# Kernel tuning notes

Hardware: AMD Instinct MI355X
Metric: run time of the kernel (lower is better)

## Reference

```python
import jax, jax.numpy as jnp
import numpy as np

N, F_IN, HID, C, E = 100000, 1024, 16, 64, 3200000
BN_EPS = 1e-5


def setup_inputs() -> dict:
    key = jax.random.key(0)
    ks = jax.random.split(key, 8)
    x = jax.random.normal(ks[0], (N, F_IN), jnp.float32)
    edge_index = jax.random.randint(ks[1], (2, E), 0, N, dtype=jnp.int32)
    w1 = jax.random.normal(ks[2], (F_IN, HID), jnp.float32) / np.float32(np.sqrt(F_IN))
    b1 = jnp.zeros((HID,), jnp.float32)
    w2 = jax.random.normal(ks[3], (HID, C), jnp.float32) / np.float32(np.sqrt(HID))
    b2 = jnp.zeros((C,), jnp.float32)
    mlp_w = jax.random.normal(ks[4], (C, C), jnp.float32) / np.float32(np.sqrt(C))
    mlp_b = jnp.zeros((C,), jnp.float32)
    bn_gamma = jnp.ones((C,), jnp.float32)
    bn_beta = jnp.zeros((C,), jnp.float32)
    # per-node channel weight param, xavier_normal_ init on shape (N, 1)
    xavier_std = np.float32(np.sqrt(2.0 / (N + 1)))
    weight_raw = jax.random.normal(ks[5], (N, 1), jnp.float32) * xavier_std
    return {"x": x, "edge_index": edge_index, "w1": w1, "b1": b1, "w2": w2,
            "b2": b2, "mlp_w": mlp_w, "mlp_b": mlp_b, "bn_gamma": bn_gamma,
            "bn_beta": bn_beta, "weight_raw": weight_raw}


def _gcn_norm(edge_index, n):
    # PyG GCNConv default: add self-loops, norm = deg^-1/2[src] * deg^-1/2[dst]
    loop = jnp.arange(n, dtype=edge_index.dtype)
    src = jnp.concatenate([edge_index[0], loop])
    dst = jnp.concatenate([edge_index[1], loop])
    deg = jax.ops.segment_sum(jnp.ones_like(dst, dtype=jnp.float32), dst, num_segments=n)
    dis = jax.lax.rsqrt(jnp.maximum(deg, 1.0))  # deg >= 1 with self-loops
    norm = dis[src] * dis[dst]
    return src, dst, norm


def _gcn_conv(h, src, dst, norm, w, b, n):
    h = h @ w                              # [N, out] dense transform first
    msg = h[src] * norm[:, None]           # gather + scale per edge
    out = jax.ops.segment_sum(msg, dst, num_segments=n)  # scatter-add
    return out + b


def reference(x, edge_index, w1, b1, w2, b2, mlp_w, mlp_b, bn_gamma, bn_beta, weight_raw):
    n = x.shape[0]
    src, dst, norm = _gcn_norm(edge_index, n)
    h = _gcn_conv(x, src, dst, norm, w1, b1, n)
    h = jax.nn.relu(h)                     # dropout is identity in eval mode
    h = _gcn_conv(h, src, dst, norm, w2, b2, n)
    h = jax.nn.log_softmax(h, axis=1)
    h = jnp.exp(weight_raw) * h            # exp(xavier param) channel weight
    h = h @ mlp_w + mlp_b                  # final MLP (C*1 -> C)
    mean = jnp.mean(h, axis=0)
    var = jnp.mean(jnp.square(h - mean), axis=0)  # biased var, BN training stats
    h = (h - mean) * jax.lax.rsqrt(var + BN_EPS) * bn_gamma + bn_beta
    return jax.nn.log_softmax(h, axis=1)
```

## Files before the change

kernel.cpp:

```cpp
#include <hip/hip_runtime.h>
#include <math.h>

#define NN   100000
#define FIN  1024
#define HIDN 16
#define CCH  64
#define EE   3200000
#define BNEPS 1e-5f
#define NB   ((NN + 255) / 256)
#define NPART 8
#define PSZ  (NN / NPART)

__global__ __launch_bounds__(256) void k_hist(const int* __restrict__ ei,
                                              unsigned* __restrict__ deg) {
  int p = blockIdx.x & 7;
  int blk = blockIdx.x >> 3;
  int nblk = gridDim.x >> 3;
  int lo = p * PSZ, hi = lo + PSZ;
  for (int e = blk * 256 + threadIdx.x; e < EE; e += nblk * 256) {
    int d = ei[EE + e];
    if (d >= lo && d < hi) atomicAdd(&deg[d], 1u);
  }
}

__global__ __launch_bounds__(256) void k_scan_part(const unsigned* __restrict__ deg,
                                                   unsigned* __restrict__ exc,
                                                   unsigned* __restrict__ bsum) {
  __shared__ unsigned s[256];
  int t = threadIdx.x, i = blockIdx.x * 256 + t;
  unsigned v = (i < NN) ? deg[i] : 0u;
  s[t] = v;
  __syncthreads();
#pragma unroll
  for (int off = 1; off < 256; off <<= 1) {
    unsigned u = (t >= off) ? s[t - off] : 0u;
    __syncthreads();
    s[t] += u;
    __syncthreads();
  }
  if (i < NN) exc[i] = s[t] - v;
  if (t == 255) bsum[blockIdx.x] = s[255];
}

__global__ __launch_bounds__(512) void k_scan_boff(const unsigned* __restrict__ bsum,
                                                   unsigned* __restrict__ boff) {
  __shared__ unsigned s[512];
  int t = threadIdx.x;
  unsigned v = (t < NB) ? bsum[t] : 0u;
  s[t] = v;
  __syncthreads();
#pragma unroll
  for (int off = 1; off < 512; off <<= 1) {
    unsigned u = (t >= off) ? s[t - off] : 0u;
    __syncthreads();
    s[t] += u;
    __syncthreads();
  }
  if (t < NB) boff[t] = s[t] - v;
}

__global__ __launch_bounds__(256) void k_scan_final(const unsigned* __restrict__ exc,
                                                    const unsigned* __restrict__ boff,
                                                    const unsigned* __restrict__ deg,
                                                    int* __restrict__ rowptr,
                                                    int* __restrict__ cur,
                                                    float* __restrict__ dis) {
  int i = blockIdx.x * 256 + threadIdx.x;
  if (i < NN) {
    int r = (int)(boff[i >> 8] + exc[i]);
    rowptr[i] = r;
    cur[i] = r;
    dis[i] = rsqrtf((float)(deg[i] + 1u));
  } else if (i == NN) {
    rowptr[NN] = EE;
  }
}

__global__ __launch_bounds__(256) void k_place(const int* __restrict__ ei,
                                               int* __restrict__ cur,
                                               int* __restrict__ perm) {
  int p = blockIdx.x & 7;
  int blk = blockIdx.x >> 3;
  int nblk = gridDim.x >> 3;
  int lo = p * PSZ, hi = lo + PSZ;
  for (int e = blk * 256 + threadIdx.x; e < EE; e += nblk * 256) {
    int d = ei[EE + e];
    if (d >= lo && d < hi) {
      int s = ei[e];
      int slot = atomicAdd(&cur[d], 1);
      perm[slot] = s;
    }
  }
}

#define G1_ROWS_PER_BLOCK 128
__global__ __launch_bounds__(256, 2) void k_gemm1(const float* __restrict__ x,
                                                  const float* __restrict__ w1,
                                                  const float* __restrict__ dis,
                                                  float* __restrict__ xw1s) {
  __shared__ __align__(16) float w1s[1024 * 16];
  const float4* w1v = (const float4*)w1;
  for (int idx = threadIdx.x; idx < 4096; idx += 256) {
    int k = idx >> 2, qj = idx & 3;
    int pq = qj ^ ((k >> 1) & 3);
    *(float4*)&w1s[(k << 4) + (pq << 2)] = w1v[idx];
  }
  __syncthreads();

  const int lane = threadIdx.x & 63;
  const int wave = threadIdx.x >> 6;
  const int sw = (lane >> 1) & 3;
  const int wave_row0 = blockIdx.x * G1_ROWS_PER_BLOCK + wave * 32;

  for (int g = 0; g < 8; ++g) {
    int row0 = wave_row0 + g * 4;
    if (row0 >= NN) break;
    int r0 = row0;
    int r1 = min(row0 + 1, NN - 1);
    int r2 = min(row0 + 2, NN - 1);
    int r3 = min(row0 + 3, NN - 1);

    const float* p0 = x + (size_t)r0 * FIN + lane;
    const float* p1 = x + (size_t)r1 * FIN + lane;
    const float* p2 = x + (size_t)r2 * FIN + lane;
    const float* p3 = x + (size_t)r3 * FIN + lane;

    float xa[16], xb[16], xc[16], xd[16];
#pragma unroll
    for (int i = 0; i < 16; ++i) {
      xa[i] = __builtin_nontemporal_load(p0 + i * 64);
      xb[i] = __builtin_nontemporal_load(p1 + i * 64);
      xc[i] = __builtin_nontemporal_load(p2 + i * 64);
      xd[i] = __builtin_nontemporal_load(p3 + i * 64);
    }

    float acc[64];
#pragma unroll
    for (int t = 0; t < 64; ++t) acc[t] = 0.0f;

#pragma unroll
    for (int i = 0; i < 16; ++i) {
      const float* wr = &w1s[(i * 64 + lane) << 4];
      float xv0 = xa[i], xv1 = xb[i], xv2 = xc[i], xv3 = xd[i];
#pragma unroll
      for (int q = 0; q < 4; ++q) {
        float4 wq = *(const float4*)(wr + ((q ^ sw) << 2));
        int b = q * 4;
        acc[b + 0]      += xv0 * wq.x;
        acc[b + 1]      += xv0 * wq.y;
        acc[b + 2]      += xv0 * wq.z;
        acc[b + 3]      += xv0 * wq.w;
        acc[16 + b + 0] += xv1 * wq.x;
        acc[16 + b + 1] += xv1 * wq.y;
        acc[16 + b + 2] += xv1 * wq.z;
        acc[16 + b + 3] += xv1 * wq.w;
        acc[32 + b + 0] += xv2 * wq.x;
        acc[32 + b + 1] += xv2 * wq.y;
        acc[32 + b + 2] += xv2 * wq.z;
        acc[32 + b + 3] += xv2 * wq.w;
        acc[48 + b + 0] += xv3 * wq.x;
        acc[48 + b + 1] += xv3 * wq.y;
        acc[48 + b + 2] += xv3 * wq.z;
        acc[48 + b + 3] += xv3 * wq.w;
      }
    }

#pragma unroll
    for (int o = 32; o >= 1; o >>= 1) {
      bool up = (lane & o) != 0;
#pragma unroll
      for (int t = 0; t < o; ++t) {
        float send = up ? acc[t] : acc[t + o];
        float recv = __shfl_xor(send, o, 64);
        float keep = up ? acc[t + o] : acc[t];
        acc[t] = keep + recv;
      }
    }

    int grow = row0 + (lane >> 4);
    if (grow < NN) xw1s[grow * HIDN + (lane & 15)] = acc[0] * dis[grow];
  }
}

template <int MODE>
__global__ __launch_bounds__(256) void k_agg(const int* __restrict__ rowptr,
                                             const int* __restrict__ perm,
                                             const float* __restrict__ dis,
                                             const float* __restrict__ sfs,
                                             const float* __restrict__ b1,
                                             float* __restrict__ out) {
  int g = blockIdx.x * 4 + (threadIdx.x >> 6);
  if (g >= NN) return;
  int lane = threadIdx.x & 63;
  int eo = lane >> 4;
  int j = lane & 15;
  int beg = rowptr[g], end = rowptr[g + 1];
  float acc0 = 0.0f, acc1 = 0.0f;
  int e = beg + eo;
  for (; e + 4 < end; e += 8) {
    int s0 = perm[e];
    int s1 = perm[e + 4];
    acc0 += sfs[(size_t)s0 * HIDN + j];
    acc1 += sfs[(size_t)s1 * HIDN + j];
  }
  if (e < end) acc0 += sfs[(size_t)perm[e] * HIDN + j];
  float acc = acc0 + acc1;
  acc += __shfl_xor(acc, 16, 64);
  acc += __shfl_xor(acc, 32, 64);
  if (eo == 0) {
    float di = dis[g];
    float v = di * (acc + sfs[(size_t)g * HIDN + j]);
    if (MODE == 0)
      out[(size_t)g * HIDN + j] = fmaxf(v + b1[j], 0.0f) * di;
    else
      out[(size_t)g * HIDN + j] = v;
  }
}

__global__ __launch_bounds__(256) void k_fuse2(const float* __restrict__ agg2,
                                               const float* __restrict__ w2,
                                               const float* __restrict__ b2,
                                               const float* __restrict__ mlpw,
                                               const float* __restrict__ mlpb,
                                               const float* __restrict__ wraw,
                                               float* __restrict__ out,
                                               double* __restrict__ gsum,
                                               double* __restrict__ gsq) {
  __shared__ __align__(16) float2 w2p[8 * CCH];
  __shared__ __align__(16) float2 mlpp[32 * CCH];
  __shared__ __align__(16) float avbuf[4][HIDN];
  __shared__ __align__(16) float gbuf[4][CCH];
  __shared__ double reds[256];
  __shared__ double redq[256];
  for (int idx = threadIdx.x; idx < 8 * CCH; idx += 256) {
    int k2 = idx >> 6, j = idx & 63;
    w2p[idx] = make_float2(w2[(2 * k2) * CCH + j], w2[(2 * k2 + 1) * CCH + j]);
  }
  for (int idx = threadIdx.x; idx < 32 * CCH; idx += 256) {
    int c2 = idx >> 6, j = idx & 63;
    mlpp[idx] = make_float2(mlpw[(2 * c2) * CCH + j], mlpw[(2 * c2 + 1) * CCH + j]);
  }
  __syncthreads();

  const int lane = threadIdx.x & 63;
  const int wave = threadIdx.x >> 6;
  const int j = lane;
  const float b2j = b2[j];
  const float mbj = mlpb[j];
  const int gw = blockIdx.x * 4 + wave;
  const int nw = gridDim.x * 4;

  double sum = 0.0, sq = 0.0;
  for (int i = gw; i < NN; i += nw) {
    float av = agg2[(size_t)i * HIDN + (lane & 15)];
    if (lane < HIDN) avbuf[wave][lane] = av;

    float2 h2p = make_float2(0.0f, 0.0f);
#pragma unroll
    for (int k2 = 0; k2 < 8; ++k2) {
      float2 a = *(const float2*)&avbuf[wave][2 * k2];
      float2 wv = w2p[k2 * CCH + j];
      h2p.x = fmaf(a.x, wv.x, h2p.x);
      h2p.y = fmaf(a.y, wv.y, h2p.y);
    }
    float h2 = h2p.x + h2p.y + b2j;

    float mx = h2;
#pragma unroll
    for (int o = 32; o >= 1; o >>= 1) mx = fmaxf(mx, __shfl_xor(mx, o, 64));
    float ex = __expf(h2 - mx);
    float se = ex;
#pragma unroll
    for (int o = 32; o >= 1; o >>= 1) se += __shfl_xor(se, o, 64);
    float lsm = h2 - mx - __logf(se);

    float gg = __expf(wraw[i]) * lsm;
    gbuf[wave][j] = gg;

    float2 mp = make_float2(0.0f, 0.0f);
#pragma unroll
    for (int c2 = 0; c2 < 32; ++c2) {
      float2 gv = *(const float2*)&gbuf[wave][2 * c2];
      float2 wv = mlpp[c2 * CCH + j];
      mp.x = fmaf(gv.x, wv.x, mp.x);
      mp.y = fmaf(gv.y, wv.y, mp.y);
    }
    float m = mp.x + mp.y + mbj;

    out[(size_t)i * CCH + j] = m;
    sum += (double)m;
    sq = fma((double)m, (double)m, sq);
  }

  reds[threadIdx.x] = sum;
  redq[threadIdx.x] = sq;
  __syncthreads();
  if (threadIdx.x < 64) {
    double s = reds[threadIdx.x] + reds[threadIdx.x + 64] +
               reds[threadIdx.x + 128] + reds[threadIdx.x + 192];
    double q = redq[threadIdx.x] + redq[threadIdx.x + 64] +
               redq[threadIdx.x + 128] + redq[threadIdx.x + 192];
    atomicAdd(&gsum[threadIdx.x], s);
    atomicAdd(&gsq[threadIdx.x], q);
  }
}

__global__ void k_stats(const double* __restrict__ gsum,
                        const double* __restrict__ gsq,
                        const float* __restrict__ gamma,
                        const float* __restrict__ beta,
                        float* __restrict__ bnp) {
  int j = threadIdx.x;
  if (j >= CCH) return;
  const double inv_n = 1.0 / (double)NN;
  double mean = gsum[j] * inv_n;
  double var = gsq[j] * inv_n - mean * mean;
  float sc = (float)(rsqrt(var + (double)BNEPS)) * gamma[j];
  bnp[j] = (float)mean;
  bnp[CCH + j] = sc;
  bnp[2 * CCH + j] = beta[j];
}

__global__ __launch_bounds__(256) void k_out(float* __restrict__ out,
                                             const float* __restrict__ bnp) {
  const int lane = threadIdx.x & 63;
  const int wave = threadIdx.x >> 6;
  const int j = lane;
  const float mean = bnp[j];
  const float sc = bnp[CCH + j];
  const float bt = bnp[2 * CCH + j];
  const int gw = blockIdx.x * 4 + wave;
  const int nw = gridDim.x * 4;
  for (int i = gw; i < NN; i += nw) {
    float m = out[(size_t)i * CCH + j];
    float y = fmaf(m - mean, sc, bt);
    float mx = y;
#pragma unroll
    for (int o = 32; o >= 1; o >>= 1) mx = fmaxf(mx, __shfl_xor(mx, o, 64));
    float ex = __expf(y - mx);
    float se = ex;
#pragma unroll
    for (int o = 32; o >= 1; o >>= 1) se += __shfl_xor(se, o, 64);
    out[(size_t)i * CCH + j] = y - mx - __logf(se);
  }
}

extern "C" void kernel_launch(void* const* d_in, const int* in_sizes, int n_in,
                              void* d_out, int out_size, void* d_ws, size_t ws_size,
                              hipStream_t stream) {
  const float* x     = (const float*)d_in[0];
  const int*   ei    = (const int*)d_in[1];
  const float* w1    = (const float*)d_in[2];
  const float* b1    = (const float*)d_in[3];
  const float* w2    = (const float*)d_in[4];
  const float* b2    = (const float*)d_in[5];
  const float* mlpw  = (const float*)d_in[6];
  const float* mlpb  = (const float*)d_in[7];
  const float* gamma = (const float*)d_in[8];
  const float* beta  = (const float*)d_in[9];
  const float* wraw  = (const float*)d_in[10];
  float* out = (float*)d_out;

  char* w = (char*)d_ws;
  size_t off = 0;
  auto take = [&](size_t bytes) -> void* {
    void* p = w + off;
    off = (off + bytes + 255) & ~(size_t)255;
    return p;
  };
  unsigned* deg    = (unsigned*)take((size_t)NN * 4);
  float*    dis    = (float*)take((size_t)NN * 4);
  unsigned* exc    = (unsigned*)take((size_t)NN * 4);
  unsigned* bsum   = (unsigned*)take((size_t)NB * 4);
  unsigned* boff   = (unsigned*)take((size_t)NB * 4);
  int*      rowptr = (int*)take((size_t)(NN + 1) * 4);
  int*      cur    = (int*)take((size_t)NN * 4);
  int*      perm   = (int*)take((size_t)EE * 4);
  float*    xw1s   = (float*)take((size_t)NN * HIDN * 4);
  float*    rh1s   = (float*)take((size_t)NN * HIDN * 4);
  float*    agg2   = (float*)take((size_t)NN * HIDN * 4);
  double*   gsum   = (double*)take(CCH * 8);
  double*   gsq    = (double*)take(CCH * 8);
  float*    bnp    = (float*)take(3 * CCH * 4);
  (void)ws_size; (void)n_in; (void)in_sizes; (void)out_size;

  hipMemsetAsync(deg, 0, (size_t)NN * 4, stream);
  hipMemsetAsync(gsum, 0, CCH * 8, stream);
  hipMemsetAsync(gsq, 0, CCH * 8, stream);

  k_hist<<<2048, 256, 0, stream>>>(ei, deg);
  k_scan_part<<<NB, 256, 0, stream>>>(deg, exc, bsum);
  k_scan_boff<<<1, 512, 0, stream>>>(bsum, boff);
  k_scan_final<<<(NN + 256) / 256 + 1, 256, 0, stream>>>(exc, boff, deg, rowptr, cur, dis);
  k_place<<<2048, 256, 0, stream>>>(ei, cur, perm);

  k_gemm1<<<(NN + G1_ROWS_PER_BLOCK - 1) / G1_ROWS_PER_BLOCK, 256, 0, stream>>>(
      x, w1, dis, xw1s);
  k_agg<0><<<(NN + 3) / 4, 256, 0, stream>>>(rowptr, perm, dis, xw1s, b1, rh1s);
  k_agg<1><<<(NN + 3) / 4, 256, 0, stream>>>(rowptr, perm, dis, rh1s, b1, agg2);
  k_fuse2<<<2048, 256, 0, stream>>>(agg2, w2, b2, mlpw, mlpb, wraw, out, gsum, gsq);
  k_stats<<<1, 64, 0, stream>>>(gsum, gsq, gamma, beta, bnp);
  k_out<<<1024, 256, 0, stream>>>(out, bnp);
}
```

Baseline: 593.6 us.

## Split gemm1 K dimension into two passes, unroll aggregation loop, enlarge grids

The dense x@w1 kernel is split into two launches, each covering half of the 1024-wide K dimension. Each launch uses half the LDS for weights and half the register-held x values. The first writes partial sums to a new buffer, and the second adds them and applies the degree scaling. The gather-aggregation loop is unrolled to four independent accumulators for more memory-level parallelism, and the fuse2 and output kernels get larger grids. The split adds a partial-sum round trip and an extra launch, and x is still read once overall, in two strided halves.

```diff
diff --git a/kernel.cpp b/kernel.cpp
--- a/kernel.cpp
+++ b/kernel.cpp
@@ -94,16 +94,18 @@
 }
 
 #define G1_ROWS_PER_BLOCK 128
+template <int HALF>
 __global__ __launch_bounds__(256, 2) void k_gemm1(const float* __restrict__ x,
                                                   const float* __restrict__ w1,
                                                   const float* __restrict__ dis,
+                                                  float* __restrict__ part,
                                                   float* __restrict__ xw1s) {
-  __shared__ __align__(16) float w1s[1024 * 16];
+  __shared__ __align__(16) float w1s[512 * 16];
   const float4* w1v = (const float4*)w1;
-  for (int idx = threadIdx.x; idx < 4096; idx += 256) {
+  for (int idx = threadIdx.x; idx < 2048; idx += 256) {
     int k = idx >> 2, qj = idx & 3;
     int pq = qj ^ ((k >> 1) & 3);
-    *(float4*)&w1s[(k << 4) + (pq << 2)] = w1v[idx];
+    *(float4*)&w1s[(k << 4) + (pq << 2)] = w1v[HALF * 2048 + idx];
   }
   __syncthreads();
 
@@ -120,14 +122,14 @@
     int r2 = min(row0 + 2, NN - 1);
     int r3 = min(row0 + 3, NN - 1);
 
-    const float* p0 = x + (size_t)r0 * FIN + lane;
-    const float* p1 = x + (size_t)r1 * FIN + lane;
-    const float* p2 = x + (size_t)r2 * FIN + lane;
-    const float* p3 = x + (size_t)r3 * FIN + lane;
-
-    float xa[16], xb[16], xc[16], xd[16];
-#pragma unroll
-    for (int i = 0; i < 16; ++i) {
+    const float* p0 = x + (size_t)r0 * FIN + HALF * 512 + lane;
+    const float* p1 = x + (size_t)r1 * FIN + HALF * 512 + lane;
+    const float* p2 = x + (size_t)r2 * FIN + HALF * 512 + lane;
+    const float* p3 = x + (size_t)r3 * FIN + HALF * 512 + lane;
+
+    float xa[8], xb[8], xc[8], xd[8];
+#pragma unroll
+    for (int i = 0; i < 8; ++i) {
       xa[i] = __builtin_nontemporal_load(p0 + i * 64);
       xb[i] = __builtin_nontemporal_load(p1 + i * 64);
       xc[i] = __builtin_nontemporal_load(p2 + i * 64);
@@ -139,7 +141,7 @@
     for (int t = 0; t < 64; ++t) acc[t] = 0.0f;
 
 #pragma unroll
-    for (int i = 0; i < 16; ++i) {
+    for (int i = 0; i < 8; ++i) {
       const float* wr = &w1s[(i * 64 + lane) << 4];
       float xv0 = xa[i], xv1 = xb[i], xv2 = xc[i], xv3 = xd[i];
 #pragma unroll
@@ -178,7 +180,14 @@
     }
 
     int grow = row0 + (lane >> 4);
-    if (grow < NN) xw1s[grow * HIDN + (lane & 15)] = acc[0] * dis[grow];
+    if (grow < NN) {
+      int oidx = grow * HIDN + (lane & 15);
+      if (HALF == 0) {
+        part[oidx] = acc[0];
+      } else {
+        xw1s[oidx] = (part[oidx] + acc[0]) * dis[grow];
+      }
+    }
   }
 }
 
@@ -195,16 +204,20 @@
   int eo = lane >> 4;
   int j = lane & 15;
   int beg = rowptr[g], end = rowptr[g + 1];
-  float acc0 = 0.0f, acc1 = 0.0f;
+  float acc0 = 0.0f, acc1 = 0.0f, acc2 = 0.0f, acc3 = 0.0f;
   int e = beg + eo;
-  for (; e + 4 < end; e += 8) {
+  for (; e + 12 < end; e += 16) {
     int s0 = perm[e];
     int s1 = perm[e + 4];
+    int s2 = perm[e + 8];
+    int s3 = perm[e + 12];
     acc0 += sfs[(size_t)s0 * HIDN + j];
     acc1 += sfs[(size_t)s1 * HIDN + j];
-  }
-  if (e < end) acc0 += sfs[(size_t)perm[e] * HIDN + j];
-  float acc = acc0 + acc1;
+    acc2 += sfs[(size_t)s2 * HIDN + j];
+    acc3 += sfs[(size_t)s3 * HIDN + j];
+  }
+  for (; e < end; e += 4) acc0 += sfs[(size_t)perm[e] * HIDN + j];
+  float acc = (acc0 + acc1) + (acc2 + acc3);
   acc += __shfl_xor(acc, 16, 64);
   acc += __shfl_xor(acc, 32, 64);
   if (eo == 0) {
@@ -376,6 +389,7 @@
   int*      rowptr = (int*)take((size_t)(NN + 1) * 4);
   int*      cur    = (int*)take((size_t)NN * 4);
   int*      perm   = (int*)take((size_t)EE * 4);
+  float*    partb  = (float*)take((size_t)NN * HIDN * 4);
   float*    xw1s   = (float*)take((size_t)NN * HIDN * 4);
   float*    rh1s   = (float*)take((size_t)NN * HIDN * 4);
   float*    agg2   = (float*)take((size_t)NN * HIDN * 4);
@@ -394,11 +408,13 @@
   k_scan_final<<<(NN + 256) / 256 + 1, 256, 0, stream>>>(exc, boff, deg, rowptr, cur, dis);
   k_place<<<2048, 256, 0, stream>>>(ei, cur, perm);
 
-  k_gemm1<<<(NN + G1_ROWS_PER_BLOCK - 1) / G1_ROWS_PER_BLOCK, 256, 0, stream>>>(
-      x, w1, dis, xw1s);
+  const int g1grid = (NN + G1_ROWS_PER_BLOCK - 1) / G1_ROWS_PER_BLOCK;
+  k_gemm1<0><<<g1grid, 256, 0, stream>>>(x, w1, dis, partb, xw1s);
+  k_gemm1<1><<<g1grid, 256, 0, stream>>>(x, w1, dis, partb, xw1s);
+
   k_agg<0><<<(NN + 3) / 4, 256, 0, stream>>>(rowptr, perm, dis, xw1s, b1, rh1s);
   k_agg<1><<<(NN + 3) / 4, 256, 0, stream>>>(rowptr, perm, dis, rh1s, b1, agg2);
-  k_fuse2<<<2048, 256, 0, stream>>>(agg2, w2, b2, mlpw, mlpb, wraw, out, gsum, gsq);
+  k_fuse2<<<4096, 256, 0, stream>>>(agg2, w2, b2, mlpw, mlpb, wraw, out, gsum, gsq);
   k_stats<<<1, 64, 0, stream>>>(gsum, gsq, gamma, beta, bnp);
-  k_out<<<1024, 256, 0, stream>>>(out, bnp);
-}
+  k_out<<<2048, 256, 0, stream>>>(out, bnp);
+}
```

Result: slower. 622.4 us (+4.8%).

## Pad w1 LDS layout, unroll aggregation gathers deeper, enlarge fuse/out grids

Applied to the files above, without the earlier changes.

The first GEMM now stores w1 in shared memory with a row stride of 17 floats and reads scalars instead of XOR-swizzled float4 vectors. This avoids bank conflicts through padding but issues four times as many LDS reads. The aggregation kernel now keeps four independent gather accumulators per lane instead of two, so more irregular loads are in flight, and its tail loop handles the remainder. The grids for k_fuse2 and k_out are doubled to add parallelism.

```diff
diff --git a/kernel.cpp b/kernel.cpp
--- a/kernel.cpp
+++ b/kernel.cpp
@@ -94,22 +94,20 @@
 }
 
 #define G1_ROWS_PER_BLOCK 128
+#define W1LD 17
 __global__ __launch_bounds__(256, 2) void k_gemm1(const float* __restrict__ x,
                                                   const float* __restrict__ w1,
                                                   const float* __restrict__ dis,
                                                   float* __restrict__ xw1s) {
-  __shared__ __align__(16) float w1s[1024 * 16];
-  const float4* w1v = (const float4*)w1;
-  for (int idx = threadIdx.x; idx < 4096; idx += 256) {
-    int k = idx >> 2, qj = idx & 3;
-    int pq = qj ^ ((k >> 1) & 3);
-    *(float4*)&w1s[(k << 4) + (pq << 2)] = w1v[idx];
+  __shared__ float w1s[1024 * W1LD];
+  for (int idx = threadIdx.x; idx < 1024 * 16; idx += 256) {
+    int k = idx >> 4, j = idx & 15;
+    w1s[k * W1LD + j] = w1[idx];
   }
   __syncthreads();
 
   const int lane = threadIdx.x & 63;
   const int wave = threadIdx.x >> 6;
-  const int sw = (lane >> 1) & 3;
   const int wave_row0 = blockIdx.x * G1_ROWS_PER_BLOCK + wave * 32;
 
   for (int g = 0; g < 8; ++g) {
@@ -140,28 +138,15 @@
 
 #pragma unroll
     for (int i = 0; i < 16; ++i) {
-      const float* wr = &w1s[(i * 64 + lane) << 4];
+      const float* wr = &w1s[(i * 64 + lane) * W1LD];
       float xv0 = xa[i], xv1 = xb[i], xv2 = xc[i], xv3 = xd[i];
 #pragma unroll
-      for (int q = 0; q < 4; ++q) {
-        float4 wq = *(const float4*)(wr + ((q ^ sw) << 2));
-        int b = q * 4;
-        acc[b + 0]      += xv0 * wq.x;
-        acc[b + 1]      += xv0 * wq.y;
-        acc[b + 2]      += xv0 * wq.z;
-        acc[b + 3]      += xv0 * wq.w;
-        acc[16 + b + 0] += xv1 * wq.x;
-        acc[16 + b + 1] += xv1 * wq.y;
-        acc[16 + b + 2] += xv1 * wq.z;
-        acc[16 + b + 3] += xv1 * wq.w;
-        acc[32 + b + 0] += xv2 * wq.x;
-        acc[32 + b + 1] += xv2 * wq.y;
-        acc[32 + b + 2] += xv2 * wq.z;
-        acc[32 + b + 3] += xv2 * wq.w;
-        acc[48 + b + 0] += xv3 * wq.x;
-        acc[48 + b + 1] += xv3 * wq.y;
-        acc[48 + b + 2] += xv3 * wq.z;
-        acc[48 + b + 3] += xv3 * wq.w;
+      for (int j = 0; j < 16; ++j) {
+        float wv = wr[j];
+        acc[j]      += xv0 * wv;
+        acc[16 + j] += xv1 * wv;
+        acc[32 + j] += xv2 * wv;
+        acc[48 + j] += xv3 * wv;
       }
     }
 
@@ -195,16 +180,20 @@
   int eo = lane >> 4;
   int j = lane & 15;
   int beg = rowptr[g], end = rowptr[g + 1];
-  float acc0 = 0.0f, acc1 = 0.0f;
+  float acc0 = 0.0f, acc1 = 0.0f, acc2 = 0.0f, acc3 = 0.0f;
   int e = beg + eo;
-  for (; e + 4 < end; e += 8) {
+  for (; e + 12 < end; e += 16) {
     int s0 = perm[e];
     int s1 = perm[e + 4];
+    int s2 = perm[e + 8];
+    int s3 = perm[e + 12];
     acc0 += sfs[(size_t)s0 * HIDN + j];
     acc1 += sfs[(size_t)s1 * HIDN + j];
-  }
-  if (e < end) acc0 += sfs[(size_t)perm[e] * HIDN + j];
-  float acc = acc0 + acc1;
+    acc2 += sfs[(size_t)s2 * HIDN + j];
+    acc3 += sfs[(size_t)s3 * HIDN + j];
+  }
+  for (; e < end; e += 4) acc0 += sfs[(size_t)perm[e] * HIDN + j];
+  float acc = (acc0 + acc1) + (acc2 + acc3);
   acc += __shfl_xor(acc, 16, 64);
   acc += __shfl_xor(acc, 32, 64);
   if (eo == 0) {
@@ -398,7 +387,7 @@
       x, w1, dis, xw1s);
   k_agg<0><<<(NN + 3) / 4, 256, 0, stream>>>(rowptr, perm, dis, xw1s, b1, rh1s);
   k_agg<1><<<(NN + 3) / 4, 256, 0, stream>>>(rowptr, perm, dis, rh1s, b1, agg2);
-  k_fuse2<<<2048, 256, 0, stream>>>(agg2, w2, b2, mlpw, mlpb, wraw, out, gsum, gsq);
+  k_fuse2<<<4096, 256, 0, stream>>>(agg2, w2, b2, mlpw, mlpb, wraw, out, gsum, gsq);
   k_stats<<<1, 64, 0, stream>>>(gsum, gsq, gamma, beta, bnp);
-  k_out<<<1024, 256, 0, stream>>>(out, bnp);
-}
+  k_out<<<2048, 256, 0, stream>>>(out, bnp);
+}
```

Result: slower. 619.6 us (+4.4%).
